# Kernel tuning notes

Measured on AMD Instinct MI355X. Metric: run time of the kernel, lower is better.

The kernel has to match this reference:

```python
import jax, jax.numpy as jnp
import numpy as np

B, N, M = 2, 10000, 320000
F, LAT, STY = 64, 128, 128
HEADS, HID = 4, 32
OUT = 3 + F  # 67
NEG = 0.2    # leaky relu slope (both activation and GAT attention)
EPS = 1e-5


def leaky(x):
    return jax.nn.leaky_relu(x, NEG)


def layer_norm(x, g, b):
    mu = jnp.mean(x, axis=-1, keepdims=True)
    var = jnp.var(x, axis=-1, keepdims=True)
    return (x - mu) * jax.lax.rsqrt(var + EPS) * g + b


def gat_conv(h, src, dst, W, a_src, a_dst, bias, heads, out_dim, n_nodes, concat):
    # h: [n, in]; W: [in, heads*out_dim]; a_*: [heads, out_dim]
    ht = (h @ W).reshape(n_nodes, heads, out_dim)
    al_s = jnp.einsum('nhd,hd->nh', ht, a_src)  # source contribution
    al_d = jnp.einsum('nhd,hd->nh', ht, a_dst)  # destination contribution
    e = leaky(al_s[src] + al_d[dst])            # [E, heads]
    emax = jax.ops.segment_max(e, dst, num_segments=n_nodes)
    ex = jnp.exp(e - emax[dst])
    denom = jax.ops.segment_sum(ex, dst, num_segments=n_nodes)
    alpha = ex / (denom[dst] + 1e-16)           # scatter-softmax over in-edges
    msg = ht[src] * alpha[:, :, None]           # [E, heads, out_dim]
    agg = jax.ops.segment_sum(msg, dst, num_segments=n_nodes)
    agg = agg.reshape(n_nodes, heads * out_dim) if concat else agg.mean(axis=1)
    return agg + bias


def setup_inputs():
    key = jax.random.key(0)
    ks = jax.random.split(key, 20)
    g = lambda i, sh, s=0.05: jax.random.normal(ks[i], sh, jnp.float32) * s
    d = {}
    d['z'] = g(0, (B, LAT), 1.0)
    d['x'] = g(1, (N, F), 1.0)
    d['pos'] = g(2, (N, 3), 1.0)
    d['edge_index'] = jax.random.randint(ks[3], (2, M), 0, N)
    d['w1'] = g(4, (LAT, 256)); d['b1'] = jnp.zeros((256,), jnp.float32)
    d['w2'] = g(5, (256, 512)); d['b2'] = jnp.zeros((512,), jnp.float32)
    d['w3'] = g(6, (512, STY)); d['b3'] = jnp.zeros((STY,), jnp.float32)
    in0 = F + STY
    d['gw0'] = g(7, (in0, HEADS * HID)); d['ga0s'] = g(8, (HEADS, HID)); d['ga0d'] = g(9, (HEADS, HID)); d['gb0'] = jnp.zeros((HEADS * HID,), jnp.float32)
    in1 = HEADS * HID
    d['gw1'] = g(10, (in1, HEADS * HID)); d['ga1s'] = g(11, (HEADS, HID)); d['ga1d'] = g(12, (HEADS, HID)); d['gb1'] = jnp.zeros((HEADS * HID,), jnp.float32)
    d['gw2'] = g(13, (in1, OUT)); d['ga2s'] = g(14, (1, OUT)); d['ga2d'] = g(15, (1, OUT)); d['gb2'] = jnp.zeros((OUT,), jnp.float32)
    d['ln0_g'] = jnp.ones((in1,), jnp.float32); d['ln0_b'] = jnp.zeros((in1,), jnp.float32)
    d['ln1_g'] = jnp.ones((in1,), jnp.float32); d['ln1_b'] = jnp.zeros((in1,), jnp.float32)
    return d


def _batched_edges(edge_index):
    # replicate template edges B times with node-id offsets, then add self-loops
    ei = jnp.concatenate([edge_index + b * N for b in range(B)], axis=1)
    sl = jnp.arange(B * N, dtype=edge_index.dtype)
    src = jnp.concatenate([ei[0], sl])
    dst = jnp.concatenate([ei[1], sl])
    return src, dst


def _forward(z, x, pos, src, dst,
             w1, b1, w2, b2, w3, b3,
             gw0, ga0s, ga0d, gb0, gw1, ga1s, ga1d, gb1, gw2, ga2s, ga2d, gb2,
             ln0_g, ln0_b, ln1_g, ln1_b):
    n_tot = B * N
    # style MLP
    s = leaky(z @ w1 + b1)
    s = leaky(s @ w2 + b2)
    style = s @ w3 + b3                               # [B, STY]
    xb = jnp.tile(x, (B, 1))                          # [B*N, F]
    pb = jnp.tile(pos, (B, 1))                        # [B*N, 3]
    style_exp = jnp.repeat(style, N, axis=0)          # [B*N, STY]
    H = jnp.concatenate([xb, style_exp], axis=1)
    H = gat_conv(H, src, dst, gw0, ga0s, ga0d, gb0, HEADS, HID, n_tot, True)
    H = leaky(layer_norm(H, ln0_g, ln0_b))
    H = gat_conv(H, src, dst, gw1, ga1s, ga1d, gb1, HEADS, HID, n_tot, True)
    H = leaky(layer_norm(H, ln1_g, ln1_b))
    H_out = gat_conv(H, src, dst, gw2, ga2s, ga2d, gb2, 1, OUT, n_tot, False)
    p_new = pb + H_out[:, :3]
    f_new = xb + H_out[:, 3:]
    return f_new, p_new


def reference(z, x, pos, edge_index,
              w1, b1, w2, b2, w3, b3,
              gw0, ga0s, ga0d, gb0, gw1, ga1s, ga1d, gb1, gw2, ga2s, ga2d, gb2,
              ln0_g, ln0_b, ln1_g, ln1_b):
    src, dst = _batched_edges(edge_index)
    return _forward(z, x, pos, src, dst,
                    w1, b1, w2, b2, w3, b3,
                    gw0, ga0s, ga0d, gb0, gw1, ga1s, ga1d, gb1, gw2, ga2s, ga2d, gb2,
                    ln0_g, ln0_b, ln1_g, ln1_b)
```

## Files before the change

### kernel.cpp

```cpp
#include <hip/hip_runtime.h>
#include <hip/hip_bf16.h>

#define DEV_INLINE __device__ __forceinline__

constexpr int Nn   = 10000;
constexpr int NT   = 20000;
constexpr int Me   = 320000;
constexpr int STRIDE = 96;
constexpr float NEG = 0.2f;

typedef float  f32x4  __attribute__((ext_vector_type(4)));
typedef float  f32x2  __attribute__((ext_vector_type(2)));
typedef short  bf16x8 __attribute__((ext_vector_type(8)));

DEV_INLINE float leaky(float x){ return x >= 0.f ? x : NEG*x; }

DEV_INLINE ushort f2bf(float v){
  __hip_bfloat16 h = __float2bfloat16(v);
  return *reinterpret_cast<ushort*>(&h);
}
DEV_INLINE float bf2f(ushort u){
  uint x = ((uint)u) << 16;
  return __uint_as_float(x);
}

DEV_INLINE unsigned char f2f8(float v){
#if __has_builtin(__builtin_amdgcn_cvt_pk_fp8_f32)
  return (unsigned char)(__builtin_amdgcn_cvt_pk_fp8_f32(v, v, 0, false) & 0xFF);
#else
  uint u = __float_as_uint(v);
  uint s = (u >> 24) & 0x80u;
  uint au = u & 0x7FFFFFFFu;
  if (au >= 0x43E00000u) return (unsigned char)(s | 0x7Eu);
  uint au2 = au + 0x0007FFFFu + ((au >> 20) & 1u);
  int e = (int)(au2 >> 23) - 120;
  if (e <= 0) return (unsigned char)s;
  uint r = ((uint)e << 3) | ((au2 >> 20) & 7u);
  if (r >= 0x7Fu) r = 0x7Eu;
  return (unsigned char)(s | r);
#endif
}
template<bool HI>
DEV_INLINE f32x2 f8x2f(uint p){
#if __has_builtin(__builtin_amdgcn_cvt_pk_f32_fp8)
  return __builtin_amdgcn_cvt_pk_f32_fp8((int)p, HI);
#else
  uint b0 = HI ? ((p >> 16) & 0xFFu) : (p & 0xFFu);
  uint b1 = HI ? ((p >> 24) & 0xFFu) : ((p >> 8) & 0xFFu);
  f32x2 r;
  uint m0 = b0 & 0x7Fu, m1 = b1 & 0x7Fu;
  uint f0 = (m0 >= 8) ? ((m0 + 960u) << 20) : 0u;
  uint f1 = (m1 >= 8) ? ((m1 + 960u) << 20) : 0u;
  f0 |= (b0 & 0x80u) << 24; f1 |= (b1 & 0x80u) << 24;
  r.x = __uint_as_float(f0); r.y = __uint_as_float(f1);
  return r;
#endif
}

DEV_INLINE float sel4(float4 w, int h){
  return h < 2 ? (h == 0 ? w.x : w.y) : (h == 2 ? w.z : w.w);
}
DEV_INLINE float red16(float v){
  v += __shfl_xor(v, 1); v += __shfl_xor(v, 2);
  v += __shfl_xor(v, 4); v += __shfl_xor(v, 8);
  return v;
}
DEV_INLINE float red32(float v){
  v += __shfl_xor(v, 1); v += __shfl_xor(v, 2);
  v += __shfl_xor(v, 4); v += __shfl_xor(v, 8);
  v += __shfl_xor(v, 16);
  return v;
}

template<int K>
__global__ __launch_bounds__(256) void k_mlp(const float* __restrict__ in,
    const float* __restrict__ W, const float* __restrict__ bias,
    float* __restrict__ out, int OD, int doAct, int mlpBlocks,
    int* __restrict__ zbuf, int zn, int zblk,
    const float* __restrict__ xsrc, ushort* __restrict__ xdst, int xn4, int xblk,
    const float* __restrict__ w3, const float* __restrict__ G,
    float* __restrict__ M, const float* __restrict__ b3, float* __restrict__ bG,
    int mblk){
  if ((int)blockIdx.x >= mlpBlocks){
    int b2 = blockIdx.x - mlpBlocks;
    if (b2 < zblk){
      int i = b2*256 + threadIdx.x;
      if (i < zn) zbuf[i] = 0;
    } else if ((b2 -= zblk) < xblk){
      int i4 = b2*256 + threadIdx.x;
      if (i4 < xn4){
        float4 v = ((const float4*)xsrc)[i4];
        ushort4 o;
        o.x = f2bf(v.x); o.y = f2bf(v.y); o.z = f2bf(v.z); o.w = f2bf(v.w);
        ((ushort4*)xdst)[i4] = o;
      }
    } else if ((b2 -= xblk) < mblk){
      int k = b2*2 + (threadIdx.x >> 7);
      int j = threadIdx.x & 127;
      float a = 0.f;
      for (int m=0; m<128; m++) a += w3[k*128 + m] * G[m*128 + j];
      M[(size_t)k*128 + j] = a;
    } else {
      if (threadIdx.x < 128){
        int j = threadIdx.x;
        float a = 0.f;
        for (int m=0; m<128; m++) a += b3[m] * G[m*128 + j];
        bG[j] = a;
      }
    }
    return;
  }
  int wave = threadIdx.x >> 6, lane = threadIdx.x & 63;
  int o = blockIdx.x*4 + wave;
  if (o >= 2*OD) return;
  int b = (o >= OD) ? 1 : 0;
  int j = o - b*OD;
  const float* __restrict__ ip = in + b*K;
  float acc = 0.f;
  #pragma unroll 2
  for (int k = lane; k < K; k += 64) acc += ip[k] * W[(size_t)k*OD + j];
  #pragma unroll
  for (int off = 32; off; off >>= 1) acc += __shfl_xor(acc, off);
  if (lane == 0){
    float v = acc + (bias ? bias[j] : 0.f);
    out[o] = doAct ? leaky(v) : v;
  }
}

__global__ __launch_bounds__(256) void k_ht0_mfma(const ushort* __restrict__ xb,
    const float* __restrict__ gw0, const float* __restrict__ styleW0,
    const float* __restrict__ a_s, const float* __restrict__ a_d,
    unsigned char* __restrict__ ht0, float* __restrict__ alS, float* __restrict__ alD,
    int mbBlocks, const int* __restrict__ eidx, int* __restrict__ cnt,
    ushort* __restrict__ slot){
  if ((int)blockIdx.x >= mbBlocks){
    int e = (blockIdx.x - mbBlocks)*256 + threadIdx.x;
    if (e < Me){
      int s = eidx[e], d = eidx[Me + e];
      int p = atomicAdd(&cnt[d], 1);
      if (p < STRIDE) slot[(size_t)d*STRIDE + p] = (ushort)s;
    }
    return;
  }
  __shared__ ushort bt[128*64];
  __shared__ float stycS[2][4], stycD[2][4];
  int t = threadIdx.x;
  int wid = t >> 6, lane = t & 63, l15 = lane & 15, g = lane >> 4;
  int mbase = blockIdx.x*128 + wid*32;

  bf16x8 afr[2][2];
  #pragma unroll
  for (int mf=0; mf<2; mf++){
    int row = mbase + mf*16 + l15;
    int rc = row < Nn ? row : Nn-1;
    const ushort* ap = xb + (size_t)rc*64 + g*8;
    #pragma unroll
    for (int ks=0; ks<2; ks++)
      afr[mf][ks] = *(const bf16x8*)(ap + ks*32);
  }

  for (int idx = t; idx < 64*128; idx += 256){
    int k = idx >> 7, c = idx & 127;
    uint byte = ((uint)(c*64 + k) << 1) ^ ((uint)(c&7) << 4);
    *(ushort*)((char*)bt + byte) = f2bf(gw0[k*128 + c]);
  }

  if (t < 128){
    int c = t, h = c >> 5;
    float as_c = a_s[c], ad_c = a_d[c];
    float s0 = styleW0[c], s1 = styleW0[128 + c];
    float v0s = red32(s0*as_c), v0d = red32(s0*ad_c);
    float v1s = red32(s1*as_c), v1d = red32(s1*ad_c);
    if ((lane & 31) == 0){
      stycS[0][h] = v0s; stycD[0][h] = v0d;
      stycS[1][h] = v1s; stycD[1][h] = v1d;
    }
  }
  __syncthreads();

  f32x4 acc[2][8];
  #pragma unroll
  for (int mf=0; mf<2; mf++)
    #pragma unroll
    for (int nf=0; nf<8; nf++) acc[mf][nf] = (f32x4){0.f,0.f,0.f,0.f};

  #pragma unroll
  for (int ks=0; ks<2; ks++){
    int kb = ks*32 + g*8;
    bf16x8 bfr[8];
    #pragma unroll
    for (int nf=0; nf<8; nf++){
      int c = nf*16 + l15;
      uint byte = ((uint)(c*64 + kb) << 1) ^ ((uint)(c&7) << 4);
      bfr[nf] = *(const bf16x8*)((const char*)bt + byte);
    }
    #pragma unroll
    for (int mf=0; mf<2; mf++)
      #pragma unroll
      for (int nf=0; nf<8; nf++)
        acc[mf][nf] = __builtin_amdgcn_mfma_f32_16x16x32_bf16(
            afr[mf][ks], bfr[nf], acc[mf][nf], 0, 0, 0);
  }

  float sw0[8], sw1[8], as_v[8], ad_v[8];
  #pragma unroll
  for (int nf=0; nf<8; nf++){
    int c = nf*16 + l15;
    sw0[nf] = styleW0[c]; sw1[nf] = styleW0[128 + c];
    as_v[nf] = a_s[c];    ad_v[nf] = a_d[c];
  }
  #pragma unroll
  for (int mf=0; mf<2; mf++){
    int rbase = mbase + mf*16 + g*4;
    #pragma unroll
    for (int r=0; r<4; r++){
      int row = rbase + r;
      bool ok = (row < Nn);
      #pragma unroll
      for (int nf=0; nf<8; nf++){
        int c = nf*16 + l15;
        if (ok){
          float v = acc[mf][nf][r];
          ht0[(size_t)row*128 + c]      = f2f8(v + sw0[nf]);
          ht0[(size_t)(Nn+row)*128 + c] = f2f8(v + sw1[nf]);
        }
      }
      float ps0 = acc[mf][0][r]*as_v[0] + acc[mf][1][r]*as_v[1];
      float ps1 = acc[mf][2][r]*as_v[2] + acc[mf][3][r]*as_v[3];
      float ps2 = acc[mf][4][r]*as_v[4] + acc[mf][5][r]*as_v[5];
      float ps3 = acc[mf][6][r]*as_v[6] + acc[mf][7][r]*as_v[7];
      float pd0 = acc[mf][0][r]*ad_v[0] + acc[mf][1][r]*ad_v[1];
      float pd1 = acc[mf][2][r]*ad_v[2] + acc[mf][3][r]*ad_v[3];
      float pd2 = acc[mf][4][r]*ad_v[4] + acc[mf][5][r]*ad_v[5];
      float pd3 = acc[mf][6][r]*ad_v[6] + acc[mf][7][r]*ad_v[7];
      ps0 = red16(ps0); ps1 = red16(ps1); ps2 = red16(ps2); ps3 = red16(ps3);
      pd0 = red16(pd0); pd1 = red16(pd1); pd2 = red16(pd2); pd3 = red16(pd3);
      if (l15 == 0 && ok){
        *(float4*)(alS + (size_t)row*4) = make_float4(
            ps0 + stycS[0][0], ps1 + stycS[0][1], ps2 + stycS[0][2], ps3 + stycS[0][3]);
        *(float4*)(alD + (size_t)row*4) = make_float4(
            pd0 + stycD[0][0], pd1 + stycD[0][1], pd2 + stycD[0][2], pd3 + stycD[0][3]);
        *(float4*)(alS + (size_t)(Nn+row)*4) = make_float4(
            ps0 + stycS[1][0], ps1 + stycS[1][1], ps2 + stycS[1][2], ps3 + stycS[1][3]);
        *(float4*)(alD + (size_t)(Nn+row)*4) = make_float4(
            pd0 + stycD[1][0], pd1 + stycD[1][1], pd2 + stycD[1][2], pd3 + stycD[1][3]);
      }
    }
  }
}

template<int NCOL, int LDO, int NF, int NHEAD>
__global__ __launch_bounds__(256) void k_mm_mfma(const ushort* __restrict__ A,
    const float* __restrict__ W, unsigned char* __restrict__ out,
    const float* __restrict__ a_s, const float* __restrict__ a_d,
    float* __restrict__ alS, float* __restrict__ alD, int M){
  constexpr int NCOLP = NF*16;
  __shared__ ushort bt[NCOLP*128];
  int t = threadIdx.x;
  int wid = t >> 6, lane = t & 63, l15 = lane & 15, g = lane >> 4;
  int mbase = blockIdx.x*128 + wid*32;

  bf16x8 afr[2][4];
  #pragma unroll
  for (int mf=0; mf<2; mf++){
    int row = mbase + mf*16 + l15;
    int rc = row < M ? row : M-1;
    const ushort* ap = A + (size_t)rc*128 + g*8;
    #pragma unroll
    for (int ks=0; ks<4; ks++)
      afr[mf][ks] = *(const bf16x8*)(ap + ks*32);
  }

  for (int idx = t; idx < 128*NCOLP; idx += 256){
    int k = idx / NCOLP, c = idx % NCOLP;
    float v = (c < NCOL) ? W[k*NCOL + c] : 0.f;
    uint byte = ((uint)(c*128 + k) << 1) ^ ((uint)(c&7) << 4);
    *(ushort*)((char*)bt + byte) = f2bf(v);
  }
  __syncthreads();

  f32x4 acc[2][NF];
  #pragma unroll
  for (int mf=0; mf<2; mf++)
    #pragma unroll
    for (int nf=0; nf<NF; nf++) acc[mf][nf] = (f32x4){0.f,0.f,0.f,0.f};

  #pragma unroll
  for (int ks=0; ks<4; ks++){
    int kb = ks*32 + g*8;
    bf16x8 bfr[NF];
    #pragma unroll
    for (int nf=0; nf<NF; nf++){
      int c = nf*16 + l15;
      uint byte = ((uint)(c*128 + kb) << 1) ^ ((uint)(c&7) << 4);
      bfr[nf] = *(const bf16x8*)((const char*)bt + byte);
    }
    #pragma unroll
    for (int mf=0; mf<2; mf++)
      #pragma unroll
      for (int nf=0; nf<NF; nf++)
        acc[mf][nf] = __builtin_amdgcn_mfma_f32_16x16x32_bf16(
            afr[mf][ks], bfr[nf], acc[mf][nf], 0, 0, 0);
  }

  #pragma unroll
  for (int mf=0; mf<2; mf++){
    int rbase = mbase + mf*16 + g*4;
    #pragma unroll
    for (int nf=0; nf<NF; nf++){
      int c = nf*16 + l15;
      if (c < LDO){
        #pragma unroll
        for (int r=0; r<4; r++){
          int row = rbase + r;
          if (row < M) out[(size_t)row*LDO + c] =
              (c < NCOL) ? f2f8(acc[mf][nf][r]) : (unsigned char)0;
        }
      }
    }
  }

  float as_v[NF], ad_v[NF];
  #pragma unroll
  for (int nf=0; nf<NF; nf++){
    int c = nf*16 + l15;
    as_v[nf] = (c < NCOL) ? a_s[c] : 0.f;
    ad_v[nf] = (c < NCOL) ? a_d[c] : 0.f;
  }
  #pragma unroll
  for (int mf=0; mf<2; mf++){
    #pragma unroll
    for (int r=0; r<4; r++){
      int row = mbase + mf*16 + g*4 + r;
      if constexpr (NHEAD == 4){
        float ps0 = acc[mf][0][r]*as_v[0] + acc[mf][1][r]*as_v[1];
        float ps1 = acc[mf][2][r]*as_v[2] + acc[mf][3][r]*as_v[3];
        float ps2 = acc[mf][4][r]*as_v[4] + acc[mf][5][r]*as_v[5];
        float ps3 = acc[mf][6][r]*as_v[6] + acc[mf][7][r]*as_v[7];
        float pd0 = acc[mf][0][r]*ad_v[0] + acc[mf][1][r]*ad_v[1];
        float pd1 = acc[mf][2][r]*ad_v[2] + acc[mf][3][r]*ad_v[3];
        float pd2 = acc[mf][4][r]*ad_v[4] + acc[mf][5][r]*ad_v[5];
        float pd3 = acc[mf][6][r]*ad_v[6] + acc[mf][7][r]*ad_v[7];
        ps0 = red16(ps0); ps1 = red16(ps1); ps2 = red16(ps2); ps3 = red16(ps3);
        pd0 = red16(pd0); pd1 = red16(pd1); pd2 = red16(pd2); pd3 = red16(pd3);
        if (l15 == 0 && row < M){
          *(float4*)(alS + (size_t)row*4) = make_float4(ps0, ps1, ps2, ps3);
          *(float4*)(alD + (size_t)row*4) = make_float4(pd0, pd1, pd2, pd3);
        }
      } else {
        float ps = 0.f, pd = 0.f;
        #pragma unroll
        for (int nf=0; nf<NF; nf++){
          ps += acc[mf][nf][r]*as_v[nf];
          pd += acc[mf][nf][r]*ad_v[nf];
        }
        ps = red16(ps); pd = red16(pd);
        if (l15 == 0 && row < M){
          alS[row] = ps; alD[row] = pd;
        }
      }
    }
  }
}

__global__ __launch_bounds__(256) void k_gat128(const unsigned char* __restrict__ ht,
    const float* __restrict__ alS, const float* __restrict__ alD,
    const int* __restrict__ deg, const ushort* __restrict__ slot,
    const float* __restrict__ gb, const float* __restrict__ lng,
    const float* __restrict__ lnb, ushort* __restrict__ outH, int n){
  __shared__ float wbuf[4][4][68];
  __shared__ int   sbuf[4][64];
  int wave = threadIdx.x >> 6, lane = threadIdx.x & 63;
  int dd = blockIdx.x*4 + wave;
  if (dd >= n) return;
  int tr  = (dd >= Nn) ? dd - Nn : dd;
  int off = (dd >= Nn) ? Nn : 0;
  int sub = lane >> 5, li = lane & 31;
  int c0 = li*4;
  int h  = li >> 3;
  float4 ald4 = *(const float4*)(alD + dd*4);
  int dg = deg[tr]; if (dg > STRIDE) dg = STRIDE;
  int begin = tr*STRIDE, end = begin + dg;

  float4 asl = *(const float4*)(alS + dd*4);
  float4 wsl;
  wsl.x = __expf(leaky(asl.x + ald4.x));
  wsl.y = __expf(leaky(asl.y + ald4.y));
  wsl.z = __expf(leaky(asl.z + ald4.z));
  wsl.w = __expf(leaky(asl.w + ald4.w));
  float es = sel4(wsl, h);
  float acc0=0.f, acc1=0.f, acc2=0.f, acc3=0.f, den=0.f;
  if (sub == 0){
    uint sv = *(const uint*)(ht + (size_t)dd*128 + c0);
    f32x2 lo = f8x2f<false>(sv), hi = f8x2f<true>(sv);
    den = es;
    acc0 = es * lo.x; acc1 = es * lo.y;
    acc2 = es * hi.x; acc3 = es * hi.y;
  }

  const unsigned char* __restrict__ htp = ht + c0;

  for (int j = begin; j < end; j += 64){
    int nc = min(64, end - j);
    if (lane < nc){
      int s = (int)slot[j + lane] + off;
      float4 as4 = *(const float4*)(alS + s*4);
      wbuf[wave][0][lane] = __expf(leaky(as4.x + ald4.x));
      wbuf[wave][1][lane] = __expf(leaky(as4.y + ald4.y));
      wbuf[wave][2][lane] = __expf(leaky(as4.z + ald4.z));
      wbuf[wave][3][lane] = __expf(leaky(as4.w + ald4.w));
      sbuf[wave][lane] = s;
    }
    const float* __restrict__ wh = wbuf[wave][h];
    int q = 0;
    for (; q + 8 <= nc; q += 8){
      int sv[4]; float wv[4];
      #pragma unroll
      for (int u=0;u<4;u++){ int e = q + 2*u + sub; sv[u] = sbuf[wave][e]; wv[u] = wh[e]; }
      uint hv[4];
      #pragma unroll
      for (int u=0;u<4;u++) hv[u] = *(const uint*)(htp + (size_t)sv[u]*128);
      #pragma unroll
      for (int u=0;u<4;u++){
        f32x2 lo = f8x2f<false>(hv[u]), hi = f8x2f<true>(hv[u]);
        den  += wv[u];
        acc0 += wv[u] * lo.x; acc1 += wv[u] * lo.y;
        acc2 += wv[u] * hi.x; acc3 += wv[u] * hi.y;
      }
    }
    for (; q < nc; q += 2){
      int e = q + sub;
      if (e < nc){
        int s = sbuf[wave][e];
        float w = wh[e];
        uint hv = *(const uint*)(htp + (size_t)s*128);
        f32x2 lo = f8x2f<false>(hv), hi = f8x2f<true>(hv);
        den  += w;
        acc0 += w * lo.x; acc1 += w * lo.y;
        acc2 += w * hi.x; acc3 += w * hi.y;
      }
    }
  }
  acc0 += __shfl_xor(acc0, 32); acc1 += __shfl_xor(acc1, 32);
  acc2 += __shfl_xor(acc2, 32); acc3 += __shfl_xor(acc3, 32);
  den  += __shfl_xor(den, 32);

  float idn = 1.f / (den + 1e-16f);
  float4 gbv = *(const float4*)(gb + c0);
  float v0 = acc0*idn + gbv.x;
  float v1 = acc1*idn + gbv.y;
  float v2 = acc2*idn + gbv.z;
  float v3 = acc3*idn + gbv.w;

  float sum = v0+v1+v2+v3;
  float sq  = v0*v0+v1*v1+v2*v2+v3*v3;
  sum = red32(sum); sq = red32(sq);
  float mu  = sum * (1.f/128.f);
  float var = sq  * (1.f/128.f) - mu*mu;
  float inv = rsqrtf(var + 1e-5f);
  float4 lg = *(const float4*)(lng + c0);
  float4 lb = *(const float4*)(lnb + c0);
  if (sub == 0){
    float y0 = (v0 - mu)*inv*lg.x + lb.x;
    float y1 = (v1 - mu)*inv*lg.y + lb.y;
    float y2 = (v2 - mu)*inv*lg.z + lb.z;
    float y3 = (v3 - mu)*inv*lg.w + lb.w;
    uint2 ow;
    ow.x = (uint)f2bf(leaky(y0)) | ((uint)f2bf(leaky(y1)) << 16);
    ow.y = (uint)f2bf(leaky(y2)) | ((uint)f2bf(leaky(y3)) << 16);
    *(uint2*)(outH + (size_t)dd*128 + c0) = ow;
  }
}

__global__ __launch_bounds__(256) void k_gat_out(const unsigned char* __restrict__ ht2,
    const float* __restrict__ alS, const float* __restrict__ alD,
    const int* __restrict__ deg, const ushort* __restrict__ slot,
    const float* __restrict__ gb2, const float* __restrict__ x,
    const float* __restrict__ pos, float* __restrict__ out, int n){
  __shared__ float wbuf[4][64];
  __shared__ int   sbuf[4][64];
  int wave = threadIdx.x >> 6, lane = threadIdx.x & 63;
  int dd = blockIdx.x*4 + wave;
  if (dd >= n) return;
  int tr  = (dd >= Nn) ? dd - Nn : dd;
  int off = (dd >= Nn) ? Nn : 0;
  int c0 = lane*2;
  bool act = (c0 < 67);
  float ald = alD[dd];
  int dg = deg[tr]; if (dg > STRIDE) dg = STRIDE;
  int begin = tr*STRIDE, end = begin + dg;

  float wsl = __expf(leaky(alS[dd] + ald));
  float den  = wsl;
  uint sv0 = act ? (uint)*(const ushort*)(ht2 + (size_t)dd*68 + c0) : 0u;
  f32x2 sd = f8x2f<false>(sv0);
  float acc0 = wsl * sd.x;
  float acc1 = wsl * sd.y;

  const unsigned char* __restrict__ h2p = ht2 + c0;

  for (int j = begin; j < end; j += 64){
    int nc = min(64, end - j);
    if (lane < nc){
      int s = (int)slot[j + lane] + off;
      wbuf[wave][lane] = __expf(leaky(alS[s] + ald));
      sbuf[wave][lane] = s;
    }
    int q = 0;
    for (; q + 8 <= nc; q += 8){
      int sv[8]; float wv[8];
      #pragma unroll
      for (int u=0;u<8;u++){ sv[u] = sbuf[wave][q+u]; wv[u] = wbuf[wave][q+u]; }
      uint hv[8];
      #pragma unroll
      for (int u=0;u<8;u++) hv[u] = act ? (uint)*(const ushort*)(h2p + (size_t)sv[u]*68) : 0u;
      #pragma unroll
      for (int u=0;u<8;u++){
        f32x2 d = f8x2f<false>(hv[u]);
        den  += wv[u];
        acc0 += wv[u] * d.x;
        acc1 += wv[u] * d.y;
      }
    }
    for (; q < nc; q++){
      int s = sbuf[wave][q]; float w = wbuf[wave][q];
      uint hv = act ? (uint)*(const ushort*)(h2p + (size_t)s*68) : 0u;
      f32x2 d = f8x2f<false>(hv);
      den  += w;
      acc0 += w * d.x;
      acc1 += w * d.y;
    }
  }
  if (!act) return;
  float idn = 1.f / (den + 1e-16f);
  int i = tr;
  int c1 = c0 + 1;
  float v0 = acc0*idn + gb2[c0];
  if (c0 < 3) out[NT*64 + dd*3 + c0] = pos[i*3 + c0] + v0;
  else        out[dd*64 + (c0-3)]    = x[i*64 + (c0-3)] + v0;
  if (c1 < 67){
    float v1 = acc1*idn + gb2[c1];
    if (c1 < 3) out[NT*64 + dd*3 + c1] = pos[i*3 + c1] + v1;
    else        out[dd*64 + (c1-3)]    = x[i*64 + (c1-3)] + v1;
  }
}

extern "C" void kernel_launch(void* const* d_in, const int* in_sizes, int n_in,
                              void* d_out, int out_size, void* d_ws, size_t ws_size,
                              hipStream_t stream){
  const float* z    = (const float*)d_in[0];
  const float* x    = (const float*)d_in[1];
  const float* pos  = (const float*)d_in[2];
  const int*   eidx = (const int*)  d_in[3];
  const float* w1   = (const float*)d_in[4];
  const float* b1   = (const float*)d_in[5];
  const float* w2   = (const float*)d_in[6];
  const float* b2   = (const float*)d_in[7];
  const float* w3   = (const float*)d_in[8];
  const float* b3   = (const float*)d_in[9];
  const float* gw0  = (const float*)d_in[10];
  const float* ga0s = (const float*)d_in[11];
  const float* ga0d = (const float*)d_in[12];
  const float* gb0  = (const float*)d_in[13];
  const float* gw1  = (const float*)d_in[14];
  const float* ga1s = (const float*)d_in[15];
  const float* ga1d = (const float*)d_in[16];
  const float* gb1  = (const float*)d_in[17];
  const float* gw2  = (const float*)d_in[18];
  const float* ga2s = (const float*)d_in[19];
  const float* ga2d = (const float*)d_in[20];
  const float* gb2  = (const float*)d_in[21];
  const float* ln0g = (const float*)d_in[22];
  const float* ln0b = (const float*)d_in[23];
  const float* ln1g = (const float*)d_in[24];
  const float* ln1b = (const float*)d_in[25];
  float* out = (float*)d_out;

  float* ws       = (float*)d_ws;
  float* styleW0  = ws;
  float* s1buf    = ws + 256;
  float* s2buf    = s1buf + 512;
  float* Mbuf     = s2buf + 1024;
  float* bGbuf    = Mbuf + 512*128;
  float* alS      = bGbuf + 128;
  float* alD      = alS + 80000;
  unsigned char* htA = (unsigned char*)(alD + 80000);
  ushort* htB     = (ushort*)(htA + (size_t)NT*128);
  unsigned char* ht2c = (unsigned char*)(htB + (size_t)NT*128);
  ushort* xb      = (ushort*)(ht2c + (size_t)NT*68);
  int*   cnt      = (int*)(xb + (size_t)Nn*64);
  ushort* slot    = (ushort*)(cnt + Nn);

  const float* G = gw0 + 64*128;

  const int ZB = (Nn + 255)/256;
  const int XB = (Nn*64/4 + 255)/256;
  const int MBk = 256;
  k_mlp<128><<<128 + ZB + XB + MBk + 1, 256, 0, stream>>>(
      z, w1, b1, s1buf, 256, 1, 128,
      cnt, Nn, ZB, x, xb, Nn*64/4, XB,
      w3, G, Mbuf, b3, bGbuf, MBk);
  k_mlp<256><<<256, 256, 0, stream>>>(s1buf, w2, b2, s2buf, 512, 1, 256,
      nullptr, 0, 0, nullptr, nullptr, 0, 0, nullptr, nullptr, nullptr, nullptr, nullptr, 0);
  k_mlp<512><<<64, 256, 0, stream>>>(s2buf, Mbuf, bGbuf, styleW0, 128, 0, 64,
      nullptr, 0, 0, nullptr, nullptr, 0, 0, nullptr, nullptr, nullptr, nullptr, nullptr, 0);

  const int MB0 = (Nn+127)/128;
  const int EB  = (Me+255)/256;
  k_ht0_mfma<<<MB0 + EB, 256, 0, stream>>>(xb, gw0, styleW0, ga0s, ga0d,
                                           htA, alS, alD, MB0, eidx, cnt, slot);
  k_gat128<<<(NT+3)/4, 256, 0, stream>>>(htA, alS, alD, cnt, slot,
                                         gb0, ln0g, ln0b, htB, NT);
  const int MB = (NT+127)/128;
  k_mm_mfma<128,128,8,4><<<MB, 256, 0, stream>>>(htB, gw1, htA, ga1s, ga1d, alS, alD, NT);
  k_gat128<<<(NT+3)/4, 256, 0, stream>>>(htA, alS, alD, cnt, slot,
                                         gb1, ln1g, ln1b, htB, NT);
  k_mm_mfma<67,68,5,1><<<MB, 256, 0, stream>>>(htB, gw2, ht2c, ga2s, ga2d, alS, alD, NT);
  k_gat_out<<<(NT+3)/4, 256, 0, stream>>>(ht2c, alS, alD, cnt, slot,
                                          gb2, x, pos, out, NT);
}
```

Before: 129.6 us.

## Fuse style MLP and x bf16 conversion into first GAT projection kernel

Replaces the three style-MLP launches with in-block computation: every projection block recomputes the full z→style→style·G chain in shared memory. The x-to-bf16 cast now happens on the fly during A-fragment loads, and counter zeroing moves to a small separate kernel. This removes two launches and the intermediate buffers. In exchange each of the 79 projection blocks redundantly does serial scalar matvecs (about 128×256 + 256×512 + 512×128 + 128×128 MACs per block), which lengthens each block's critical path before its MFMA work starts.

Result: slower. 164.2 us (+26.6%).

```diff
diff --git a/kernel.cpp b/kernel.cpp
--- a/kernel.cpp
+++ b/kernel.cpp
@@ -72,63 +72,17 @@
   return v;
 }
 
-template<int K>
-__global__ __launch_bounds__(256) void k_mlp(const float* __restrict__ in,
-    const float* __restrict__ W, const float* __restrict__ bias,
-    float* __restrict__ out, int OD, int doAct, int mlpBlocks,
-    int* __restrict__ zbuf, int zn, int zblk,
-    const float* __restrict__ xsrc, ushort* __restrict__ xdst, int xn4, int xblk,
-    const float* __restrict__ w3, const float* __restrict__ G,
-    float* __restrict__ M, const float* __restrict__ b3, float* __restrict__ bG,
-    int mblk){
-  if ((int)blockIdx.x >= mlpBlocks){
-    int b2 = blockIdx.x - mlpBlocks;
-    if (b2 < zblk){
-      int i = b2*256 + threadIdx.x;
-      if (i < zn) zbuf[i] = 0;
-    } else if ((b2 -= zblk) < xblk){
-      int i4 = b2*256 + threadIdx.x;
-      if (i4 < xn4){
-        float4 v = ((const float4*)xsrc)[i4];
-        ushort4 o;
-        o.x = f2bf(v.x); o.y = f2bf(v.y); o.z = f2bf(v.z); o.w = f2bf(v.w);
-        ((ushort4*)xdst)[i4] = o;
-      }
-    } else if ((b2 -= xblk) < mblk){
-      int k = b2*2 + (threadIdx.x >> 7);
-      int j = threadIdx.x & 127;
-      float a = 0.f;
-      for (int m=0; m<128; m++) a += w3[k*128 + m] * G[m*128 + j];
-      M[(size_t)k*128 + j] = a;
-    } else {
-      if (threadIdx.x < 128){
-        int j = threadIdx.x;
-        float a = 0.f;
-        for (int m=0; m<128; m++) a += b3[m] * G[m*128 + j];
-        bG[j] = a;
-      }
-    }
-    return;
-  }
-  int wave = threadIdx.x >> 6, lane = threadIdx.x & 63;
-  int o = blockIdx.x*4 + wave;
-  if (o >= 2*OD) return;
-  int b = (o >= OD) ? 1 : 0;
-  int j = o - b*OD;
-  const float* __restrict__ ip = in + b*K;
-  float acc = 0.f;
-  #pragma unroll 2
-  for (int k = lane; k < K; k += 64) acc += ip[k] * W[(size_t)k*OD + j];
-  #pragma unroll
-  for (int off = 32; off; off >>= 1) acc += __shfl_xor(acc, off);
-  if (lane == 0){
-    float v = acc + (bias ? bias[j] : 0.f);
-    out[o] = doAct ? leaky(v) : v;
-  }
-}
-
-__global__ __launch_bounds__(256) void k_ht0_mfma(const ushort* __restrict__ xb,
-    const float* __restrict__ gw0, const float* __restrict__ styleW0,
+__global__ __launch_bounds__(256) void k_zero(int* __restrict__ p, int n){
+  int i = blockIdx.x*256 + threadIdx.x;
+  if (i < n) p[i] = 0;
+}
+
+__global__ __launch_bounds__(256) void k_ht0_mfma(const float* __restrict__ x,
+    const float* __restrict__ z,
+    const float* __restrict__ w1, const float* __restrict__ b1,
+    const float* __restrict__ w2, const float* __restrict__ b2,
+    const float* __restrict__ w3, const float* __restrict__ b3,
+    const float* __restrict__ gw0,
     const float* __restrict__ a_s, const float* __restrict__ a_d,
     unsigned char* __restrict__ ht0, float* __restrict__ alS, float* __restrict__ alD,
     int mbBlocks, const int* __restrict__ eidx, int* __restrict__ cnt,
@@ -142,21 +96,70 @@
     }
     return;
   }
-  __shared__ ushort bt[128*64];
-  __shared__ float stycS[2][4], stycD[2][4];
+  __shared__ char smem[16384 + 8192 + 64 + 64];
+  ushort* bt  = (ushort*)smem;
+  float* sc   = (float*)(smem + 16384);
+  float* s1b  = sc;
+  float* s2b  = sc + 512;
+  float* styb = sc + 1536;
+  float* swb  = sc + 1792;
+  float* stycS = (float*)(smem + 16384 + 8192);
+  float* stycD = stycS + 8;
+  const float* G = gw0 + 64*128;
   int t = threadIdx.x;
-  int wid = t >> 6, lane = t & 63, l15 = lane & 15, g = lane >> 4;
+  int lane = t & 63, l15 = lane & 15, g = lane >> 4;
+  int wid = t >> 6;
   int mbase = blockIdx.x*128 + wid*32;
+
+  for (int o = t; o < 512; o += 256){
+    int b = o >> 8, j = o & 255;
+    float a = b1[j];
+    for (int k = 0; k < 128; k++) a += z[b*128 + k] * w1[k*256 + j];
+    s1b[o] = leaky(a);
+  }
+  __syncthreads();
+  for (int o = t; o < 1024; o += 256){
+    int b = o >> 9, j = o & 511;
+    float a = b2[j];
+    const float* s1p = s1b + b*256;
+    for (int k = 0; k < 256; k++) a += s1p[k] * w2[(size_t)k*512 + j];
+    s2b[o] = leaky(a);
+  }
+  __syncthreads();
+  {
+    int b = t >> 7, j = t & 127;
+    float a = b3[j];
+    const float* s2p = s2b + b*512;
+    for (int k = 0; k < 512; k++) a += s2p[k] * w3[k*128 + j];
+    styb[t] = a;
+  }
+  __syncthreads();
+  {
+    int b = t >> 7, j = t & 127;
+    float a = 0.f;
+    const float* sp = styb + b*128;
+    for (int k = 0; k < 128; k++) a += sp[k] * G[k*128 + j];
+    swb[t] = a;
+  }
+  __syncthreads();
 
   bf16x8 afr[2][2];
   #pragma unroll
   for (int mf=0; mf<2; mf++){
     int row = mbase + mf*16 + l15;
     int rc = row < Nn ? row : Nn-1;
-    const ushort* ap = xb + (size_t)rc*64 + g*8;
-    #pragma unroll
-    for (int ks=0; ks<2; ks++)
-      afr[mf][ks] = *(const bf16x8*)(ap + ks*32);
+    const float* xp = x + (size_t)rc*64 + g*8;
+    #pragma unroll
+    for (int ks=0; ks<2; ks++){
+      float4 va = *(const float4*)(xp + ks*32);
+      float4 vb = *(const float4*)(xp + ks*32 + 4);
+      bf16x8 f;
+      f[0] = (short)f2bf(va.x); f[1] = (short)f2bf(va.y);
+      f[2] = (short)f2bf(va.z); f[3] = (short)f2bf(va.w);
+      f[4] = (short)f2bf(vb.x); f[5] = (short)f2bf(vb.y);
+      f[6] = (short)f2bf(vb.z); f[7] = (short)f2bf(vb.w);
+      afr[mf][ks] = f;
+    }
   }
 
   for (int idx = t; idx < 64*128; idx += 256){
@@ -168,12 +171,12 @@
   if (t < 128){
     int c = t, h = c >> 5;
     float as_c = a_s[c], ad_c = a_d[c];
-    float s0 = styleW0[c], s1 = styleW0[128 + c];
+    float s0 = swb[c], s1 = swb[128 + c];
     float v0s = red32(s0*as_c), v0d = red32(s0*ad_c);
     float v1s = red32(s1*as_c), v1d = red32(s1*ad_c);
     if ((lane & 31) == 0){
-      stycS[0][h] = v0s; stycD[0][h] = v0d;
-      stycS[1][h] = v1s; stycD[1][h] = v1d;
+      stycS[0*4+h] = v0s; stycD[0*4+h] = v0d;
+      stycS[1*4+h] = v1s; stycD[1*4+h] = v1d;
     }
   }
   __syncthreads();
@@ -206,8 +209,8 @@
   #pragma unroll
   for (int nf=0; nf<8; nf++){
     int c = nf*16 + l15;
-    sw0[nf] = styleW0[c]; sw1[nf] = styleW0[128 + c];
-    as_v[nf] = a_s[c];    ad_v[nf] = a_d[c];
+    sw0[nf] = swb[c]; sw1[nf] = swb[128 + c];
+    as_v[nf] = a_s[c]; ad_v[nf] = a_d[c];
   }
   #pragma unroll
   for (int mf=0; mf<2; mf++){
@@ -237,13 +240,13 @@
       pd0 = red16(pd0); pd1 = red16(pd1); pd2 = red16(pd2); pd3 = red16(pd3);
       if (l15 == 0 && ok){
         *(float4*)(alS + (size_t)row*4) = make_float4(
-            ps0 + stycS[0][0], ps1 + stycS[0][1], ps2 + stycS[0][2], ps3 + stycS[0][3]);
+            ps0 + stycS[0], ps1 + stycS[1], ps2 + stycS[2], ps3 + stycS[3]);
         *(float4*)(alD + (size_t)row*4) = make_float4(
-            pd0 + stycD[0][0], pd1 + stycD[0][1], pd2 + stycD[0][2], pd3 + stycD[0][3]);
+            pd0 + stycD[0], pd1 + stycD[1], pd2 + stycD[2], pd3 + stycD[3]);
         *(float4*)(alS + (size_t)(Nn+row)*4) = make_float4(
-            ps0 + stycS[1][0], ps1 + stycS[1][1], ps2 + stycS[1][2], ps3 + stycS[1][3]);
+            ps0 + stycS[4], ps1 + stycS[5], ps2 + stycS[6], ps3 + stycS[7]);
         *(float4*)(alD + (size_t)(Nn+row)*4) = make_float4(
-            pd0 + stycD[1][0], pd1 + stycD[1][1], pd2 + stycD[1][2], pd3 + stycD[1][3]);
+            pd0 + stycD[4], pd1 + stycD[5], pd2 + stycD[6], pd3 + stycD[7]);
       }
     }
   }
@@ -577,37 +580,20 @@
   float* out = (float*)d_out;
 
   float* ws       = (float*)d_ws;
-  float* styleW0  = ws;
-  float* s1buf    = ws + 256;
-  float* s2buf    = s1buf + 512;
-  float* Mbuf     = s2buf + 1024;
-  float* bGbuf    = Mbuf + 512*128;
-  float* alS      = bGbuf + 128;
+  float* alS      = ws;
   float* alD      = alS + 80000;
   unsigned char* htA = (unsigned char*)(alD + 80000);
   ushort* htB     = (ushort*)(htA + (size_t)NT*128);
   unsigned char* ht2c = (unsigned char*)(htB + (size_t)NT*128);
-  ushort* xb      = (ushort*)(ht2c + (size_t)NT*68);
-  int*   cnt      = (int*)(xb + (size_t)Nn*64);
+  int*   cnt      = (int*)(ht2c + (size_t)NT*68);
   ushort* slot    = (ushort*)(cnt + Nn);
 
-  const float* G = gw0 + 64*128;
-
-  const int ZB = (Nn + 255)/256;
-  const int XB = (Nn*64/4 + 255)/256;
-  const int MBk = 256;
-  k_mlp<128><<<128 + ZB + XB + MBk + 1, 256, 0, stream>>>(
-      z, w1, b1, s1buf, 256, 1, 128,
-      cnt, Nn, ZB, x, xb, Nn*64/4, XB,
-      w3, G, Mbuf, b3, bGbuf, MBk);
-  k_mlp<256><<<256, 256, 0, stream>>>(s1buf, w2, b2, s2buf, 512, 1, 256,
-      nullptr, 0, 0, nullptr, nullptr, 0, 0, nullptr, nullptr, nullptr, nullptr, nullptr, 0);
-  k_mlp<512><<<64, 256, 0, stream>>>(s2buf, Mbuf, bGbuf, styleW0, 128, 0, 64,
-      nullptr, 0, 0, nullptr, nullptr, 0, 0, nullptr, nullptr, nullptr, nullptr, nullptr, 0);
+  k_zero<<<(Nn+255)/256, 256, 0, stream>>>(cnt, Nn);
 
   const int MB0 = (Nn+127)/128;
   const int EB  = (Me+255)/256;
-  k_ht0_mfma<<<MB0 + EB, 256, 0, stream>>>(xb, gw0, styleW0, ga0s, ga0d,
+  k_ht0_mfma<<<MB0 + EB, 256, 0, stream>>>(x, z, w1, b1, w2, b2, w3, b3,
+                                           gw0, ga0s, ga0d,
                                            htA, alS, alD, MB0, eidx, cnt, slot);
   k_gat128<<<(NT+3)/4, 256, 0, stream>>>(htA, alS, alD, cnt, slot,
                                          gb0, ln0g, ln0b, htB, NT);
```
